# Kernel optimization log

Hardware: AMD Instinct MI355X
Metric: run time of the kernel (lower is better)

Reference implementation:

```python
import jax, jax.numpy as jnp
import numpy as np

B, N, D = 4, 4096, 1024
H = 16
DH = D // H
EPS = 1e-6


def log_map_at_origin(x, c):
    # Poincare ball -> tangent space at origin (matches torch clamps)
    sqrt_c = jnp.sqrt(jnp.maximum(c, 1e-6))
    x_norm = jnp.clip(jnp.linalg.norm(x, axis=-1, keepdims=True), 1e-6, 0.999)
    scale = jnp.arctanh(sqrt_c * x_norm) / (sqrt_c * x_norm + 1e-8)
    return scale * x


def exp_map_at_origin(v, c):
    # tangent space -> Poincare ball
    sqrt_c = jnp.sqrt(jnp.maximum(c, 1e-6))
    v_norm = jnp.clip(jnp.linalg.norm(v, axis=-1, keepdims=True), 1e-6, 15.0)
    tanh_arg = jnp.minimum(sqrt_c * v_norm, 15.0)
    return jnp.tanh(tanh_arg) / (sqrt_c * v_norm + 1e-8) * v


def setup_inputs() -> dict:
    key = jax.random.key(0)
    ks = jax.random.split(key, 9)
    s = 0.02
    return {
        "x": jax.random.normal(ks[0], (B, N, D), jnp.float32),
        "curvature": jnp.asarray(0.05, jnp.float32),  # < low_threshold -> 'linear' mode
        "Wq": jax.random.normal(ks[1], (D, D), jnp.float32) * s,
        "bq": jnp.zeros((D,), jnp.float32),
        "Wk": jax.random.normal(ks[2], (D, D), jnp.float32) * s,
        "bk": jnp.zeros((D,), jnp.float32),
        "Wv": jax.random.normal(ks[3], (D, D), jnp.float32) * s,
        "bv": jnp.zeros((D,), jnp.float32),
        "Wo": jax.random.normal(ks[4], (D, D), jnp.float32) * s,
        "bo": jnp.zeros((D,), jnp.float32),
    }


def reference(x, curvature, Wq, bq, Wk, bk, Wv, bv, Wo, bo):
    c = jnp.maximum(jnp.abs(curvature), 1e-6)
    x_tan = log_map_at_origin(x, c)  # (B,N,D)

    def proj(W, b):
        # torch nn.Linear: y = x W^T + b; split heads -> (B,H,N,Dh)
        return (x_tan @ W.T + b).reshape(B, N, H, DH).transpose(0, 2, 1, 3)

    q = proj(Wq, bq)
    k = proj(Wk, bk)
    v = proj(Wv, bv)

    # KernelFeatureMap, kernel_type='elu': phi(x) = elu(x) + 1
    phi_q = jax.nn.elu(q) + 1.0  # (B,H,N,Dh)
    phi_k = jax.nn.elu(k) + 1.0

    # Linear attention: phi(Q) (phi(K)^T V) / (phi(Q) sum_n phi(K))
    kv = jnp.einsum('bhnd,bhnf->bhfd', v, phi_k)          # (B,H,F,Dh)
    qkv = jnp.einsum('bhnf,bhfd->bhnd', phi_q, kv)        # (B,H,N,Dh)
    k_sum = phi_k.sum(axis=2)                             # (B,H,F)
    normalizer = jnp.maximum(jnp.einsum('bhnf,bhf->bhn', phi_q, k_sum), EPS)
    out = qkv / normalizer[..., None]

    out = out.transpose(0, 2, 1, 3).reshape(B, N, D)
    out = out @ Wo.T + bo
    return exp_map_at_origin(out, c)
```

## Files before the change

### kernel.cpp

```cpp
#include <hip/hip_runtime.h>
#include <cstdint>
#include <cstddef>

#define Bb 4
#define Nn 4096
#define Dd 1024
#define Hh 16
#define ROWS (Bb*Nn)

typedef unsigned short u16;
typedef float    f32x4 __attribute__((ext_vector_type(4)));
typedef _Float16 f16x8 __attribute__((ext_vector_type(8)));
typedef u16      u16x4 __attribute__((ext_vector_type(4)));
typedef u16      u16x8 __attribute__((ext_vector_type(8)));

__device__ inline u16 f2h(float f){ _Float16 h=(_Float16)f; return __builtin_bit_cast(u16,h); }
__device__ inline float h2f(u16 u){ return (float)__builtin_bit_cast(_Float16,u); }

__device__ inline void gl_lds16(const void* g, void* l){
  __builtin_amdgcn_global_load_lds(
      (const __attribute__((address_space(1))) void*)g,
      (__attribute__((address_space(3))) void*)l,
      16, 0, 0);
}

__global__ __launch_bounds__(256) void prep_k(const float* __restrict__ x,
    const float* __restrict__ curv,
    const float* __restrict__ wq, const float* __restrict__ wk,
    const float* __restrict__ wv, const float* __restrict__ wo,
    const float* __restrict__ bq, const float* __restrict__ bk,
    const float* __restrict__ bv,
    u16* __restrict__ xt, u16* __restrict__ wbf, float* __restrict__ bcat)
{
  const int tid = threadIdx.x;
  if (blockIdx.x < ROWS){
    const int row = blockIdx.x;
    const f32x4 v = ((const f32x4*)(x + (size_t)row*Dd))[tid];
    float ss = v[0]*v[0] + v[1]*v[1] + v[2]*v[2] + v[3]*v[3];
    #pragma unroll
    for (int o=32;o>0;o>>=1) ss += __shfl_down(ss, o, 64);
    __shared__ float red[4];
    if ((tid & 63) == 0) red[tid>>6] = ss;
    __syncthreads();
    const float sum = red[0]+red[1]+red[2]+red[3];
    const float c  = fmaxf(fabsf(curv[0]), 1e-6f);
    const float sc = sqrtf(fmaxf(c, 1e-6f));
    const float xn = fminf(fmaxf(sqrtf(sum), 1e-6f), 0.999f);
    const float a  = sc * xn;
    const float scale = atanhf(a) / (a + 1e-8f);
    u16x4 o;
    #pragma unroll
    for (int i=0;i<4;i++) o[i] = f2h(v[i]*scale);
    ((u16x4*)(xt + (size_t)row*Dd))[tid] = o;
  } else {
    const int idx = (blockIdx.x - ROWS)*256 + tid;
    if (idx < (1<<20)){
      const int which = idx >> 18;
      const int rem = idx & ((1<<18)-1);
      const float* src = which==0?wq:which==1?wk:which==2?wv:wo;
      const f32x4 v = ((const f32x4*)src)[rem];
      u16x4 o;
      #pragma unroll
      for (int i=0;i<4;i++) o[i]=f2h(v[i]);
      ((u16x4*)(wbf + (size_t)which*(1u<<20)))[rem] = o;
    } else {
      const int t = idx - (1<<20);
      if (t < 3072)
        bcat[t] = (t<1024) ? bq[t] : (t<2048) ? bk[t-1024] : bv[t-2048];
    }
  }
}

__global__ __launch_bounds__(256) void expmap_k(const u16* __restrict__ proj,
    const float* __restrict__ curv, float* __restrict__ out)
{
  const int row = blockIdx.x, tid = threadIdx.x;
  const u16x4 hv = ((const u16x4*)(proj + (size_t)row*Dd))[tid];
  float v[4];
  #pragma unroll
  for (int i=0;i<4;i++) v[i]=h2f(hv[i]);
  float ss = v[0]*v[0]+v[1]*v[1]+v[2]*v[2]+v[3]*v[3];
  #pragma unroll
  for (int o=32;o>0;o>>=1) ss += __shfl_down(ss,o,64);
  __shared__ float red[4];
  if ((tid&63)==0) red[tid>>6]=ss;
  __syncthreads();
  const float sum = red[0]+red[1]+red[2]+red[3];
  const float c  = fmaxf(fabsf(curv[0]),1e-6f);
  const float sc = sqrtf(fmaxf(c,1e-6f));
  const float vn = fminf(fmaxf(sqrtf(sum),1e-6f),15.0f);
  const float a  = sc*vn;
  const float scale = tanhf(fminf(a,15.0f))/(a + 1e-8f);
  f32x4 o;
  #pragma unroll
  for (int i=0;i<4;i++) o[i]=v[i]*scale;
  ((f32x4*)(out + (size_t)row*Dd))[tid]=o;
}

__global__ __launch_bounds__(512, 1) void gemm8_k(
    const u16* __restrict__ A, const u16* __restrict__ W,
    const float* __restrict__ bias,
    u16* __restrict__ out_n, u16* __restrict__ outT1, u16* __restrict__ outT2,
    int nbn, int phi_modes)
{
  __shared__ __align__(16) char smem[131072];

  const int nwg = gridDim.x;
  const int bid = blockIdx.x;
  const int wgid = (bid & 7)*(nwg >> 3) + (bid >> 3);
  const int bm = wgid / nbn, bn = wgid % nbn;
  const int bm0 = bm*256, bn0 = bn*256;

  const int tid = threadIdx.x;
  const int w = tid >> 6, lane = tid & 63;
  const int wr = w >> 2, wc = w & 3;
  const int l8 = lane >> 3, l7 = lane & 7;

  f32x4 acc[8][4];
  #pragma unroll
  for (int i=0;i<8;i++)
    #pragma unroll
    for (int j=0;j<4;j++) acc[i][j] = (f32x4)(0.f);

  int offA[2][8], offB[2][4];
  #pragma unroll
  for (int ks=0;ks<2;ks++){
    #pragma unroll
    for (int mi=0;mi<8;mi++){
      const int ar = wr*128 + mi*16 + (lane & 15);
      offA[ks][mi] = ar*128 + ((ks*64 + (lane>>4)*16) ^ ((ar & 7) << 4));
    }
    #pragma unroll
    for (int ni=0;ni<4;ni++){
      const int br = wc*64 + ni*16 + (lane & 15);
      offB[ks][ni] = 32768 + br*128 + ((ks*64 + (lane>>4)*16) ^ ((br & 7) << 4));
    }
  }
  const u16* aS[4]; const u16* wS[4]; int dOf[4];
  #pragma unroll
  for (int i=0;i<4;i++){
    const int r = w*32 + i*8 + l8;
    const int cch = l7 ^ (r & 7);
    aS[i] = A + (size_t)(bm0 + r)*Dd + cch*8;
    wS[i] = W + (size_t)(bn0 + r)*Dd + cch*8;
    dOf[i] = (w*32 + i*8)*128;
  }

  auto STAGE = [&](char* base, int kt){
    #pragma unroll
    for (int i=0;i<4;i++){
      gl_lds16(aS[i] + kt*64, base + dOf[i]);
      gl_lds16(wS[i] + kt*64, base + 32768 + dOf[i]);
    }
  };

  auto COMPUTE = [&](const char* base){
    #pragma unroll
    for (int ks=0; ks<2; ks++){
      f16x8 bf[4];
      #pragma unroll
      for (int ni=0; ni<4; ni++)
        bf[ni] = *(const f16x8*)(base + offB[ks][ni]);
      __builtin_amdgcn_s_setprio(1);
      #pragma unroll
      for (int mi=0; mi<8; mi++){
        const f16x8 af = *(const f16x8*)(base + offA[ks][mi]);
        #pragma unroll
        for (int ni=0; ni<4; ni++)
          acc[mi][ni] = __builtin_amdgcn_mfma_f32_16x16x32_f16(af, bf[ni], acc[mi][ni], 0,0,0);
      }
      __builtin_amdgcn_s_setprio(0);
    }
  };

  STAGE(smem, 0);
  __syncthreads();
  #pragma unroll
  for (int p=0; p<8; ++p){
    STAGE(smem + 65536, 2*p+1);
    COMPUTE(smem);
    __syncthreads();
    if (p < 7) STAGE(smem, 2*p+2);
    COMPUTE(smem + 65536);
    __syncthreads();
  }

  const int mode = bn0 >> 10;
  const int dophi = mode < phi_modes;
  if (mode == 1 || mode == 2){
    u16* tbuf = (mode == 1) ? outT1 : outT2;
    char* Ts = smem;
    #pragma unroll
    for (int ni=0;ni<4;ni++){
      const int lcol = wc*64 + ni*16 + (lane & 15);
      const float bs = bias[bn0 + lcol];
      #pragma unroll
      for (int mi=0;mi<8;mi++){
        const int row0 = wr*128 + mi*16 + ((lane>>4)<<2);
        #pragma unroll
        for (int r=0;r<4;r++){
          float val = acc[mi][ni][r] + bs;
          if (dophi) val = val > 0.f ? val + 1.f : __expf(val);
          const int lrow = row0 + r;
          const int bo_ = (lcol*512 + lrow*2) ^ ((lcol&7)<<4);
          *(u16*)(Ts + bo_) = f2h(val);
        }
      }
    }
    __syncthreads();
    {
      const int ch = tid & 31;
      #pragma unroll
      for (int rep=0; rep<16; ++rep){
        const int c = rep*16 + (tid>>5);
        const int bo_ = (c*512 + ch*16) ^ ((c&7)<<4);
        const int mcol = (bn0 & 1023) + c;
        const int h = mcol >> 6, f = mcol & 63;
        const int bh = ((bm0 >> 12) << 4) + h;
        u16* db = tbuf + ((size_t)(bh*64 + f))*Nn + (bm0 & 4095) + ch*8;
        *(u16x8*)db = *(const u16x8*)(Ts + bo_);
      }
    }
  } else {
    u16* Ts = (u16*)smem;
    #pragma unroll
    for (int ni=0;ni<4;ni++){
      const int col = wc*64 + ni*16 + (lane & 15);
      const float bs = bias[bn0 + col];
      #pragma unroll
      for (int mi=0;mi<8;mi++){
        const int row0 = wr*128 + mi*16 + ((lane>>4)<<2);
        #pragma unroll
        for (int r=0;r<4;r++){
          float val = acc[mi][ni][r] + bs;
          if (dophi) val = val > 0.f ? val + 1.f : __expf(val);
          const int row = row0 + r;
          const int bo_ = (row*512 + col*2) ^ ((row&7)<<4);
          *(u16*)((char*)Ts + bo_) = f2h(val);
        }
      }
    }
    __syncthreads();
    #pragma unroll
    for (int j=0;j<16;j++){
      const int row = j*16 + w*2 + (lane>>5);
      const int cb2 = (lane&31)*16;
      const int bo_ = (row*512 + cb2) ^ ((row&7)<<4);
      u16* ob = out_n + (size_t)(bm0 + row)*Dd + (bn0 & 1023) + (cb2>>1);
      *(u16x8*)ob = *(const u16x8*)((const char*)Ts + bo_);
    }
  }
}

__global__ __launch_bounds__(256) void kvmm_k(const u16* __restrict__ pkT,
    const u16* __restrict__ vT, float* __restrict__ pkv, float* __restrict__ pks)
{
  const int p = blockIdx.x, bh = blockIdx.y;
  const int tid = threadIdx.x, w = tid>>6, lane = tid&63;
  __shared__ __align__(16) char smem[65536];
  const size_t abase = (size_t)bh*64*Nn;

  f32x4 acc[5];
  #pragma unroll
  for (int i=0;i<5;i++) acc[i] = (f32x4)(0.f);
  f16x8 onesf;
  #pragma unroll
  for (int i=0;i<8;i++) onesf[i] = (_Float16)1.0f;

  auto STG = [&](int d, int sub){
    char* Ap = smem + d*32768;
    char* Bp = Ap + 16384;
    const int nbase = p*512 + sub*128;
    #pragma unroll
    for (int i=0;i<4;i++){
      const int ib = (w*4+i)*64;
      const int cj = ib + lane;
      const int f = cj>>4, ci = cj&15;
      const size_t off = abase + (size_t)f*Nn + nbase + (ci ^ (f&15))*8;
      gl_lds16(pkT + off, Ap + ib*16);
      gl_lds16(vT  + off, Bp + ib*16);
    }
  };

  auto COMPUTE = [&](int d){
    const char* Ap = smem + d*32768;
    const char* Bp = Ap + 16384;
    #pragma unroll
    for (int s=0; s<4; ++s){
      const int kb = (s*64 + (lane>>4)*16) ^ ((lane&15)<<4);
      const int fr = w*16 + (lane&15);
      const f16x8 af = *(const f16x8*)(Ap + fr*256 + kb);
      #pragma unroll
      for (int ni=0; ni<4; ni++){
        const int dr = ni*16 + (lane&15);
        const f16x8 bf = *(const f16x8*)(Bp + dr*256 + kb);
        acc[ni] = __builtin_amdgcn_mfma_f32_16x16x32_f16(af, bf, acc[ni], 0,0,0);
      }
      acc[4] = __builtin_amdgcn_mfma_f32_16x16x32_f16(af, onesf, acc[4], 0,0,0);
    }
  };

  STG(0, 0);
  __syncthreads();
  for (int sub=0; sub<4; ++sub){
    const int d = sub & 1;
    if (sub < 3) STG(d^1, sub+1);
    COMPUTE(d);
    __syncthreads();
  }

  float* o = pkv + (size_t)(bh*8+p)*4096;
  #pragma unroll
  for (int ni=0;ni<4;ni++)
    #pragma unroll
    for (int r=0;r<4;r++)
      o[(w*16 + ((lane>>4)<<2) + r)*64 + ni*16 + (lane&15)] = acc[ni][r];
  if ((lane&15)==0){
    #pragma unroll
    for (int r=0;r<4;r++)
      pks[(size_t)(bh*8+p)*64 + w*16 + ((lane>>4)<<2) + r] = acc[4][r];
  }
}

__global__ __launch_bounds__(256) void kvred_k(const float* __restrict__ pkv,
    const float* __restrict__ pks, u16* __restrict__ kvt)
{
  const int bh = blockIdx.x, tid = threadIdx.x;
  u16* basep = kvt + (size_t)bh*10240;
  #pragma unroll
  for (int i=0;i<4;i++){
    const int e = tid*16 + i*4;
    f32x4 s = (f32x4)(0.f);
    for (int p=0;p<8;p++)
      s += *(const f32x4*)&pkv[(size_t)(bh*8+p)*4096 + e];
    const int f = e>>6, dd = e&63;
    #pragma unroll
    for (int j=0;j<4;j++){
      const int r = dd+j;
      const u16 hi = f2h(s[j]);
      const int col = f ^ ((r&7)<<3);
      basep[r*64 + col] = hi;
      basep[5120 + r*64 + col] = f2h(s[j] - h2f(hi));
    }
  }
  if (tid < 64){
    float s=0.f;
    for (int p=0;p<8;p++) s += pks[(size_t)(bh*8+p)*64 + tid];
    const u16 hi = f2h(s);
    basep[64*64 + tid] = hi;
    basep[5120 + 64*64 + tid] = f2h(s - h2f(hi));
  }
  if (tid < 240){
    const int r = 65 + (tid>>4), c4 = (tid&15)*4;
    *(u16x4*)&basep[r*64 + c4] = (u16x4)(0);
    *(u16x4*)&basep[5120 + r*64 + c4] = (u16x4)(0);
  }
}

__global__ __launch_bounds__(256) void attn2_k(const u16* __restrict__ phiq,
    const u16* __restrict__ kvt, u16* __restrict__ att)
{
  const int bh = blockIdx.y, b = bh>>4, h = bh&15;
  const int tid = threadIdx.x;
  const int w = tid>>6, lane = tid&63;
  __shared__ __align__(16) u16 kvs[10240];
  __shared__ __align__(16) u16 pqs[2][64*64];

  const int l8 = lane>>3, l7 = lane&7;
  auto STAGE_P = [&](int d, int nt){
    const int n0 = (blockIdx.x*4 + nt)*64;
    const u16* qsrc = phiq + ((size_t)(b*Nn) + n0)*Dd + h*64;
    #pragma unroll
    for (int i=0;i<2;i++){
      const int r = w*16 + i*8 + l8;
      const int cch = l7 ^ (r&7);
      gl_lds16(qsrc + (size_t)r*Dd + cch*8, (char*)pqs[d] + (w*16+i*8)*128);
    }
  };

  {
    const char* src = (const char*)(kvt + (size_t)bh*10240);
    #pragma unroll
    for (int j=0;j<5;j++)
      gl_lds16(src + j*4096 + w*1024 + lane*16, (char*)kvs + j*4096 + w*1024);
    STAGE_P(0, 0);
  }
  __syncthreads();

  #pragma unroll
  for (int nt=0; nt<4; ++nt){
    const int d = nt & 1;
    if (nt < 3) STAGE_P(d^1, nt+1);
    f32x4 acc[5];
    #pragma unroll
    for (int ni=0;ni<5;ni++) acc[ni] = (f32x4)(0.f);
    #pragma unroll
    for (int ks=0; ks<2; ks++){
      const int ar = w*16 + (lane&15);
      const int acb = (ks*64 + (lane>>4)*16) ^ ((ar&7)<<4);
      const f16x8 af = *(const f16x8*)((const char*)pqs[d] + ar*128 + acb);
      #pragma unroll
      for (int ni=0; ni<5; ni++){
        const int br = ni*16 + (lane&15);
        const int bcb = (ks*64 + (lane>>4)*16) ^ ((br&7)<<4);
        const f16x8 bh_ = *(const f16x8*)((const char*)kvs + br*128 + bcb);
        const f16x8 bl_ = *(const f16x8*)((const char*)kvs + 10240 + br*128 + bcb);
        acc[ni] = __builtin_amdgcn_mfma_f32_16x16x32_f16(af, bh_, acc[ni], 0,0,0);
        acc[ni] = __builtin_amdgcn_mfma_f32_16x16x32_f16(af, bl_, acc[ni], 0,0,0);
      }
    }
    const int n0 = (blockIdx.x*4 + nt)*64;
    #pragma unroll
    for (int r=0;r<4;r++){
      const float nrm = __shfl(acc[4][r], (lane & 48), 64);
      const float inv = 1.f / fmaxf(nrm, 1e-6f);
      const int row = n0 + w*16 + ((lane>>4)<<2) + r;
      u16* ob = att + ((size_t)(b*Nn) + row)*Dd + h*64 + (lane&15);
      #pragma unroll
      for (int ni=0; ni<4; ni++)
        ob[ni*16] = f2h(acc[ni][r] * inv);
    }
    __syncthreads();
  }
}

extern "C" void kernel_launch(void* const* d_in, const int* in_sizes, int n_in,
                              void* d_out, int out_size, void* d_ws, size_t ws_size,
                              hipStream_t stream)
{
  const float* x  = (const float*)d_in[0];
  const float* cv = (const float*)d_in[1];
  const float* Wq = (const float*)d_in[2];
  const float* bq = (const float*)d_in[3];
  const float* Wk = (const float*)d_in[4];
  const float* bk = (const float*)d_in[5];
  const float* Wv = (const float*)d_in[6];
  const float* bv = (const float*)d_in[7];
  const float* Wo = (const float*)d_in[8];
  const float* bo = (const float*)d_in[9];
  float* out = (float*)d_out;
  char* ws = (char*)d_ws;
  const size_t MB = 1u<<20;
  if (ws_size < 136*MB) return;

  u16* xt     = (u16*)(ws + 0);
  u16* wbf    = (u16*)(ws + 32*MB);
  u16* phiq   = (u16*)(ws + 40*MB);
  u16* phikT  = (u16*)(ws + 72*MB);
  u16* vT     = (u16*)(ws + 104*MB);
  float* pkv  = (float*)(ws + 0);
  float* pks  = (float*)(ws + 8*MB);
  u16* kvt    = (u16*)(ws + 9*MB);
  u16* att    = (u16*)(ws + 104*MB);
  u16* proj16 = (u16*)(ws + 40*MB);
  float* bcat = out + ((size_t)out_size - 4096);

  prep_k<<<ROWS + 4108, 256, 0, stream>>>(x, cv, Wq, Wk, Wv, Wo, bq, bk, bv,
                                          xt, wbf, bcat);
  gemm8_k<<<768, 512, 0, stream>>>(xt, wbf, bcat, phiq, phikT, vT,
                                   12, 2);
  kvmm_k<<<dim3(8,64), 256, 0, stream>>>(phikT, vT, pkv, pks);
  kvred_k<<<64, 256, 0, stream>>>(pkv, pks, kvt);
  attn2_k<<<dim3(16,64), 256, 0, stream>>>(phiq, kvt, att);
  gemm8_k<<<256, 512, 0, stream>>>(att, wbf + (size_t)3*(1u<<20), bo, proj16,
                                   nullptr, nullptr, 4, 0);
  expmap_k<<<ROWS, 256, 0, stream>>>(proj16, cv, out);
}
```

Baseline: 233.3 us.

## Halve GEMM K-tile and LDS to fit two workgroups per CU, templated N tile

The projection GEMM becomes a template on N-tile width. The K tile per stage drops from 64 to 32 with a new XOR swizzle, so LDS per block halves and launch bounds allow two 512-thread workgroups per CU. The epilogue now stages output through LDS one half-tile at a time so it fits the smaller buffer. The output projection uses a 256x128 tile with 512 blocks to improve load balance. The cost is twice as many barriers per K sweep and tighter register limits, which may cause spills with 32 accumulators per thread.

```diff
diff --git a/kernel.cpp b/kernel.cpp
--- a/kernel.cpp
+++ b/kernel.cpp
@@ -97,157 +97,175 @@
   ((f32x4*)(out + (size_t)row*Dd))[tid]=o;
 }
 
-__global__ __launch_bounds__(512, 1) void gemm8_k(
+template<int NI>
+__global__ __launch_bounds__(512, 2) void gemmN_k(
     const u16* __restrict__ A, const u16* __restrict__ W,
     const float* __restrict__ bias,
     u16* __restrict__ out_n, u16* __restrict__ outT1, u16* __restrict__ outT2,
     int nbn, int phi_modes)
 {
-  __shared__ __align__(16) char smem[131072];
+  constexpr int BN   = NI*64;
+  constexpr int HALF = (256+BN)*64;
+  __shared__ __align__(16) char smem[2*HALF];
 
   const int nwg = gridDim.x;
   const int bid = blockIdx.x;
   const int wgid = (bid & 7)*(nwg >> 3) + (bid >> 3);
   const int bm = wgid / nbn, bn = wgid % nbn;
-  const int bm0 = bm*256, bn0 = bn*256;
+  const int bm0 = bm*256, bn0 = bn*BN;
 
   const int tid = threadIdx.x;
   const int w = tid >> 6, lane = tid & 63;
   const int wr = w >> 2, wc = w & 3;
-  const int l8 = lane >> 3, l7 = lane & 7;
-
-  f32x4 acc[8][4];
+
+  f32x4 acc[8][NI];
   #pragma unroll
   for (int i=0;i<8;i++)
     #pragma unroll
-    for (int j=0;j<4;j++) acc[i][j] = (f32x4)(0.f);
-
-  int offA[2][8], offB[2][4];
-  #pragma unroll
-  for (int ks=0;ks<2;ks++){
-    #pragma unroll
-    for (int mi=0;mi<8;mi++){
-      const int ar = wr*128 + mi*16 + (lane & 15);
-      offA[ks][mi] = ar*128 + ((ks*64 + (lane>>4)*16) ^ ((ar & 7) << 4));
-    }
-    #pragma unroll
-    for (int ni=0;ni<4;ni++){
-      const int br = wc*64 + ni*16 + (lane & 15);
-      offB[ks][ni] = 32768 + br*128 + ((ks*64 + (lane>>4)*16) ^ ((br & 7) << 4));
-    }
-  }
-  const u16* aS[4]; const u16* wS[4]; int dOf[4];
-  #pragma unroll
-  for (int i=0;i<4;i++){
-    const int r = w*32 + i*8 + l8;
-    const int cch = l7 ^ (r & 7);
-    aS[i] = A + (size_t)(bm0 + r)*Dd + cch*8;
-    wS[i] = W + (size_t)(bn0 + r)*Dd + cch*8;
-    dOf[i] = (w*32 + i*8)*128;
+    for (int j=0;j<NI;j++) acc[i][j] = (f32x4)(0.f);
+
+  int offA[8], offB[NI];
+  #pragma unroll
+  for (int mi=0;mi<8;mi++){
+    const int ar = wr*128 + mi*16 + (lane & 15);
+    const int key = (ar ^ (ar>>2)) & 3;
+    offA[mi] = ar*64 + (((lane>>4) ^ key) << 4);
+  }
+  #pragma unroll
+  for (int ni=0;ni<NI;ni++){
+    const int br = wc*(NI*16) + ni*16 + (lane & 15);
+    const int key = (br ^ (br>>2)) & 3;
+    offB[ni] = 16384 + br*64 + (((lane>>4) ^ key) << 4);
+  }
+  const u16* aS[2]; int dofA[2];
+  #pragma unroll
+  for (int j=0;j<2;j++){
+    const int cj = tid + j*512;
+    const int r = cj>>2, sl = cj&3;
+    const int csl = sl ^ ((r ^ (r>>2)) & 3);
+    aS[j] = A + (size_t)(bm0 + r)*Dd + csl*8;
+    dofA[j] = cj*16;
+  }
+  const u16* wS[NI/2]; int dofB[NI/2];
+  #pragma unroll
+  for (int j=0;j<NI/2;j++){
+    const int cj = tid + j*512;
+    const int r = cj>>2, sl = cj&3;
+    const int csl = sl ^ ((r ^ (r>>2)) & 3);
+    wS[j] = W + (size_t)(bn0 + r)*Dd + csl*8;
+    dofB[j] = 16384 + cj*16;
   }
 
   auto STAGE = [&](char* base, int kt){
     #pragma unroll
-    for (int i=0;i<4;i++){
-      gl_lds16(aS[i] + kt*64, base + dOf[i]);
-      gl_lds16(wS[i] + kt*64, base + 32768 + dOf[i]);
-    }
+    for (int j=0;j<2;j++) gl_lds16(aS[j] + kt*32, base + dofA[j]);
+    #pragma unroll
+    for (int j=0;j<NI/2;j++) gl_lds16(wS[j] + kt*32, base + dofB[j]);
   };
 
   auto COMPUTE = [&](const char* base){
-    #pragma unroll
-    for (int ks=0; ks<2; ks++){
-      f16x8 bf[4];
-      #pragma unroll
-      for (int ni=0; ni<4; ni++)
-        bf[ni] = *(const f16x8*)(base + offB[ks][ni]);
-      __builtin_amdgcn_s_setprio(1);
-      #pragma unroll
-      for (int mi=0; mi<8; mi++){
-        const f16x8 af = *(const f16x8*)(base + offA[ks][mi]);
-        #pragma unroll
-        for (int ni=0; ni<4; ni++)
-          acc[mi][ni] = __builtin_amdgcn_mfma_f32_16x16x32_f16(af, bf[ni], acc[mi][ni], 0,0,0);
-      }
-      __builtin_amdgcn_s_setprio(0);
-    }
+    f16x8 bf[NI];
+    #pragma unroll
+    for (int ni=0; ni<NI; ni++)
+      bf[ni] = *(const f16x8*)(base + offB[ni]);
+    __builtin_amdgcn_s_setprio(1);
+    #pragma unroll
+    for (int mi=0; mi<8; mi++){
+      const f16x8 af = *(const f16x8*)(base + offA[mi]);
+      #pragma unroll
+      for (int ni=0; ni<NI; ni++)
+        acc[mi][ni] = __builtin_amdgcn_mfma_f32_16x16x32_f16(af, bf[ni], acc[mi][ni], 0,0,0);
+    }
+    __builtin_amdgcn_s_setprio(0);
   };
 
   STAGE(smem, 0);
   __syncthreads();
   #pragma unroll
-  for (int p=0; p<8; ++p){
-    STAGE(smem + 65536, 2*p+1);
+  for (int p=0; p<16; ++p){
+    STAGE(smem + HALF, 2*p+1);
     COMPUTE(smem);
     __syncthreads();
-    if (p < 7) STAGE(smem, 2*p+2);
-    COMPUTE(smem + 65536);
+    if (p < 15) STAGE(smem, 2*p+2);
+    COMPUTE(smem + HALF);
     __syncthreads();
   }
 
   const int mode = bn0 >> 10;
   const int dophi = mode < phi_modes;
-  if (mode == 1 || mode == 2){
+  if (NI == 4 && mode >= 1){
     u16* tbuf = (mode == 1) ? outT1 : outT2;
     char* Ts = smem;
     #pragma unroll
-    for (int ni=0;ni<4;ni++){
-      const int lcol = wc*64 + ni*16 + (lane & 15);
-      const float bs = bias[bn0 + lcol];
-      #pragma unroll
-      for (int mi=0;mi<8;mi++){
-        const int row0 = wr*128 + mi*16 + ((lane>>4)<<2);
+    for (int half=0; half<2; ++half){
+      if (half) __syncthreads();
+      if (wr == half){
         #pragma unroll
-        for (int r=0;r<4;r++){
-          float val = acc[mi][ni][r] + bs;
-          if (dophi) val = val > 0.f ? val + 1.f : __expf(val);
-          const int lrow = row0 + r;
-          const int bo_ = (lcol*512 + lrow*2) ^ ((lcol&7)<<4);
-          *(u16*)(Ts + bo_) = f2h(val);
+        for (int ni=0;ni<NI;ni++){
+          const int lcol = wc*(NI*16) + ni*16 + (lane & 15);
+          const float bs = bias[bn0 + lcol];
+          #pragma unroll
+          for (int mi=0;mi<8;mi++){
+            const int rl0 = mi*16 + ((lane>>4)<<2);
+            #pragma unroll
+            for (int r=0;r<4;r++){
+              float val = acc[mi][ni][r] + bs;
+              if (dophi) val = val > 0.f ? val + 1.f : __expf(val);
+              const int rl = rl0 + r;
+              const int bo_ = (lcol*256 + rl*2) ^ ((lcol&7)<<4);
+              *(u16*)(Ts + bo_) = f2h(val);
+            }
+          }
         }
       }
-    }
-    __syncthreads();
-    {
-      const int ch = tid & 31;
-      #pragma unroll
-      for (int rep=0; rep<16; ++rep){
-        const int c = rep*16 + (tid>>5);
-        const int bo_ = (c*512 + ch*16) ^ ((c&7)<<4);
-        const int mcol = (bn0 & 1023) + c;
-        const int h = mcol >> 6, f = mcol & 63;
-        const int bh = ((bm0 >> 12) << 4) + h;
-        u16* db = tbuf + ((size_t)(bh*64 + f))*Nn + (bm0 & 4095) + ch*8;
-        *(u16x8*)db = *(const u16x8*)(Ts + bo_);
+      __syncthreads();
+      {
+        const int ch = tid & 15;
+        #pragma unroll
+        for (int rep=0; rep<8; ++rep){
+          const int c = rep*32 + (tid>>4);
+          const int bo_ = (c*256 + ch*16) ^ ((c&7)<<4);
+          const int mcol = (bn0 & 1023) + c;
+          const int h = mcol >> 6, f = mcol & 63;
+          const int bh = ((bm0 >> 12) << 4) + h;
+          u16* db = tbuf + ((size_t)(bh*64 + f))*Nn + (bm0 & 4095) + half*128 + ch*8;
+          *(u16x8*)db = *(const u16x8*)(Ts + bo_);
+        }
       }
     }
   } else {
     u16* Ts = (u16*)smem;
     #pragma unroll
-    for (int ni=0;ni<4;ni++){
-      const int col = wc*64 + ni*16 + (lane & 15);
-      const float bs = bias[bn0 + col];
-      #pragma unroll
-      for (int mi=0;mi<8;mi++){
-        const int row0 = wr*128 + mi*16 + ((lane>>4)<<2);
+    for (int half=0; half<2; ++half){
+      if (half) __syncthreads();
+      if (wr == half){
         #pragma unroll
-        for (int r=0;r<4;r++){
-          float val = acc[mi][ni][r] + bs;
-          if (dophi) val = val > 0.f ? val + 1.f : __expf(val);
-          const int row = row0 + r;
-          const int bo_ = (row*512 + col*2) ^ ((row&7)<<4);
-          *(u16*)((char*)Ts + bo_) = f2h(val);
+        for (int ni=0;ni<NI;ni++){
+          const int col = wc*(NI*16) + ni*16 + (lane & 15);
+          const float bs = bias[bn0 + col];
+          #pragma unroll
+          for (int mi=0;mi<8;mi++){
+            const int rl0 = mi*16 + ((lane>>4)<<2);
+            #pragma unroll
+            for (int r=0;r<4;r++){
+              float val = acc[mi][ni][r] + bs;
+              if (dophi) val = val > 0.f ? val + 1.f : __expf(val);
+              const int rl = rl0 + r;
+              const int bo_ = (rl*(BN*2) + col*2) ^ ((rl&7)<<4);
+              *(u16*)((char*)Ts + bo_) = f2h(val);
+            }
+          }
         }
       }
-    }
-    __syncthreads();
-    #pragma unroll
-    for (int j=0;j<16;j++){
-      const int row = j*16 + w*2 + (lane>>5);
-      const int cb2 = (lane&31)*16;
-      const int bo_ = (row*512 + cb2) ^ ((row&7)<<4);
-      u16* ob = out_n + (size_t)(bm0 + row)*Dd + (bn0 & 1023) + (cb2>>1);
-      *(u16x8*)ob = *(const u16x8*)((const char*)Ts + bo_);
+      __syncthreads();
+      #pragma unroll
+      for (int t=0; t<NI*2; ++t){
+        const int c = tid + t*512;
+        const int rl = c / (BN/8), wch = c % (BN/8);
+        const int bo_ = (rl*(BN*2) + wch*16) ^ ((rl&7)<<4);
+        u16* ob = out_n + (size_t)(bm0 + half*128 + rl)*Dd + (bn0 & 1023) + wch*8;
+        *(u16x8*)ob = *(const u16x8*)((const char*)Ts + bo_);
+      }
     }
   }
 }
@@ -457,12 +475,12 @@
 
   prep_k<<<ROWS + 4108, 256, 0, stream>>>(x, cv, Wq, Wk, Wv, Wo, bq, bk, bv,
                                           xt, wbf, bcat);
-  gemm8_k<<<768, 512, 0, stream>>>(xt, wbf, bcat, phiq, phikT, vT,
-                                   12, 2);
+  gemmN_k<4><<<768, 512, 0, stream>>>(xt, wbf, bcat, phiq, phikT, vT,
+                                      12, 2);
   kvmm_k<<<dim3(8,64), 256, 0, stream>>>(phikT, vT, pkv, pks);
   kvred_k<<<64, 256, 0, stream>>>(pkv, pks, kvt);
   attn2_k<<<dim3(16,64), 256, 0, stream>>>(phiq, kvt, att);
-  gemm8_k<<<256, 512, 0, stream>>>(att, wbf + (size_t)3*(1u<<20), bo, proj16,
-                                   nullptr, nullptr, 4, 0);
+  gemmN_k<2><<<512, 512, 0, stream>>>(att, wbf + (size_t)3*(1u<<20), bo, proj16,
+                                      nullptr, nullptr, 8, 0);
   expmap_k<<<ROWS, 256, 0, stream>>>(proj16, cv, out);
 }
```

Measured after the change: 267.0 us. 1.14x slower.

## Add single-buffered half-LDS QKV GEMM variant to fit two workgroups per CU

Applied to the files above, without the earlier changes.

Adds a QKV projection GEMM that uses 64KB of LDS with a single buffer instead of 128KB double-buffered, and sets launch bounds to two workgroups per CU. Latency is meant to be hidden by running two resident workgroups rather than by software pipelining. The epilogue is split into two halves by wave row so the transpose staging fits in the smaller LDS. The output-projection GEMM keeps the old double-buffered kernel with the phi and transpose paths stripped. Risks: more register pressure under the two-block bound, which could cause spills of the 128-float accumulator, plus extra barriers and no overlap of loads with compute inside a block.

```diff
diff --git a/kernel.cpp b/kernel.cpp
--- a/kernel.cpp
+++ b/kernel.cpp
@@ -97,13 +97,13 @@
   ((f32x4*)(out + (size_t)row*Dd))[tid]=o;
 }
 
-__global__ __launch_bounds__(512, 1) void gemm8_k(
+__global__ __launch_bounds__(512, 2) void gemmS_k(
     const u16* __restrict__ A, const u16* __restrict__ W,
     const float* __restrict__ bias,
     u16* __restrict__ out_n, u16* __restrict__ outT1, u16* __restrict__ outT2,
     int nbn, int phi_modes)
 {
-  __shared__ __align__(16) char smem[131072];
+  __shared__ __align__(16) char smem[65536];
 
   const int nwg = gridDim.x;
   const int bid = blockIdx.x;
@@ -146,6 +146,168 @@
     dOf[i] = (w*32 + i*8)*128;
   }
 
+  auto STAGE = [&](int kt){
+    #pragma unroll
+    for (int i=0;i<4;i++){
+      gl_lds16(aS[i] + kt*64, smem + dOf[i]);
+      gl_lds16(wS[i] + kt*64, smem + 32768 + dOf[i]);
+    }
+  };
+
+  auto COMPUTE = [&](){
+    #pragma unroll
+    for (int ks=0; ks<2; ks++){
+      f16x8 bf[4];
+      #pragma unroll
+      for (int ni=0; ni<4; ni++)
+        bf[ni] = *(const f16x8*)(smem + offB[ks][ni]);
+      __builtin_amdgcn_s_setprio(1);
+      #pragma unroll
+      for (int mi=0; mi<8; mi++){
+        const f16x8 af = *(const f16x8*)(smem + offA[ks][mi]);
+        #pragma unroll
+        for (int ni=0; ni<4; ni++)
+          acc[mi][ni] = __builtin_amdgcn_mfma_f32_16x16x32_f16(af, bf[ni], acc[mi][ni], 0,0,0);
+      }
+      __builtin_amdgcn_s_setprio(0);
+    }
+  };
+
+  #pragma unroll
+  for (int kt=0; kt<16; ++kt){
+    STAGE(kt);
+    __syncthreads();
+    COMPUTE();
+    __syncthreads();
+  }
+
+  const int mode = bn0 >> 10;
+  const int dophi = mode < phi_modes;
+  if (mode >= 1){
+    u16* tbuf = (mode == 1) ? outT1 : outT2;
+    char* Ts = smem;
+    #pragma unroll
+    for (int half=0; half<2; ++half){
+      if (half) __syncthreads();
+      if (wr == half){
+        #pragma unroll
+        for (int ni=0;ni<4;ni++){
+          const int lcol = wc*64 + ni*16 + (lane & 15);
+          const float bs = bias[bn0 + lcol];
+          #pragma unroll
+          for (int mi=0;mi<8;mi++){
+            const int rl0 = mi*16 + ((lane>>4)<<2);
+            #pragma unroll
+            for (int r=0;r<4;r++){
+              float val = acc[mi][ni][r] + bs;
+              if (dophi) val = val > 0.f ? val + 1.f : __expf(val);
+              const int rl = rl0 + r;
+              const int bo_ = (lcol*256 + rl*2) ^ ((lcol&7)<<4);
+              *(u16*)(Ts + bo_) = f2h(val);
+            }
+          }
+        }
+      }
+      __syncthreads();
+      {
+        const int ch = tid & 15;
+        #pragma unroll
+        for (int rep=0; rep<8; ++rep){
+          const int c = rep*32 + (tid>>4);
+          const int bo_ = (c*256 + ch*16) ^ ((c&7)<<4);
+          const int mcol = (bn0 & 1023) + c;
+          const int h = mcol >> 6, f = mcol & 63;
+          const int bh = ((bm0 >> 12) << 4) + h;
+          u16* db = tbuf + ((size_t)(bh*64 + f))*Nn + (bm0 & 4095) + half*128 + ch*8;
+          *(u16x8*)db = *(const u16x8*)(Ts + bo_);
+        }
+      }
+    }
+  } else {
+    u16* Ts = (u16*)smem;
+    #pragma unroll
+    for (int half=0; half<2; ++half){
+      if (half) __syncthreads();
+      if (wr == half){
+        #pragma unroll
+        for (int ni=0;ni<4;ni++){
+          const int col = wc*64 + ni*16 + (lane & 15);
+          const float bs = bias[bn0 + col];
+          #pragma unroll
+          for (int mi=0;mi<8;mi++){
+            const int rl0 = mi*16 + ((lane>>4)<<2);
+            #pragma unroll
+            for (int r=0;r<4;r++){
+              float val = acc[mi][ni][r] + bs;
+              if (dophi) val = val > 0.f ? val + 1.f : __expf(val);
+              const int rl = rl0 + r;
+              const int bo_ = (rl*512 + col*2) ^ ((rl&7)<<4);
+              *(u16*)((char*)Ts + bo_) = f2h(val);
+            }
+          }
+        }
+      }
+      __syncthreads();
+      #pragma unroll
+      for (int t=0; t<8; ++t){
+        const int c = tid + t*512;
+        const int rl = c >> 5, wch = c & 31;
+        const int bo_ = (rl*512 + wch*16) ^ ((rl&7)<<4);
+        u16* ob = out_n + (size_t)(bm0 + half*128 + rl)*Dd + (bn0 & 1023) + wch*8;
+        *(u16x8*)ob = *(const u16x8*)((const char*)Ts + bo_);
+      }
+    }
+  }
+}
+
+__global__ __launch_bounds__(512, 1) void gemm8_k(
+    const u16* __restrict__ A, const u16* __restrict__ W,
+    const float* __restrict__ bias,
+    u16* __restrict__ out_n, int nbn)
+{
+  __shared__ __align__(16) char smem[131072];
+
+  const int nwg = gridDim.x;
+  const int bid = blockIdx.x;
+  const int wgid = (bid & 7)*(nwg >> 3) + (bid >> 3);
+  const int bm = wgid / nbn, bn = wgid % nbn;
+  const int bm0 = bm*256, bn0 = bn*256;
+
+  const int tid = threadIdx.x;
+  const int w = tid >> 6, lane = tid & 63;
+  const int wr = w >> 2, wc = w & 3;
+  const int l8 = lane >> 3, l7 = lane & 7;
+
+  f32x4 acc[8][4];
+  #pragma unroll
+  for (int i=0;i<8;i++)
+    #pragma unroll
+    for (int j=0;j<4;j++) acc[i][j] = (f32x4)(0.f);
+
+  int offA[2][8], offB[2][4];
+  #pragma unroll
+  for (int ks=0;ks<2;ks++){
+    #pragma unroll
+    for (int mi=0;mi<8;mi++){
+      const int ar = wr*128 + mi*16 + (lane & 15);
+      offA[ks][mi] = ar*128 + ((ks*64 + (lane>>4)*16) ^ ((ar & 7) << 4));
+    }
+    #pragma unroll
+    for (int ni=0;ni<4;ni++){
+      const int br = wc*64 + ni*16 + (lane & 15);
+      offB[ks][ni] = 32768 + br*128 + ((ks*64 + (lane>>4)*16) ^ ((br & 7) << 4));
+    }
+  }
+  const u16* aS[4]; const u16* wS[4]; int dOf[4];
+  #pragma unroll
+  for (int i=0;i<4;i++){
+    const int r = w*32 + i*8 + l8;
+    const int cch = l7 ^ (r & 7);
+    aS[i] = A + (size_t)(bm0 + r)*Dd + cch*8;
+    wS[i] = W + (size_t)(bn0 + r)*Dd + cch*8;
+    dOf[i] = (w*32 + i*8)*128;
+  }
+
   auto STAGE = [&](char* base, int kt){
     #pragma unroll
     for (int i=0;i<4;i++){
@@ -185,70 +347,31 @@
     __syncthreads();
   }
 
-  const int mode = bn0 >> 10;
-  const int dophi = mode < phi_modes;
-  if (mode == 1 || mode == 2){
-    u16* tbuf = (mode == 1) ? outT1 : outT2;
-    char* Ts = smem;
-    #pragma unroll
-    for (int ni=0;ni<4;ni++){
-      const int lcol = wc*64 + ni*16 + (lane & 15);
-      const float bs = bias[bn0 + lcol];
-      #pragma unroll
-      for (int mi=0;mi<8;mi++){
-        const int row0 = wr*128 + mi*16 + ((lane>>4)<<2);
-        #pragma unroll
-        for (int r=0;r<4;r++){
-          float val = acc[mi][ni][r] + bs;
-          if (dophi) val = val > 0.f ? val + 1.f : __expf(val);
-          const int lrow = row0 + r;
-          const int bo_ = (lcol*512 + lrow*2) ^ ((lcol&7)<<4);
-          *(u16*)(Ts + bo_) = f2h(val);
-        }
-      }
-    }
-    __syncthreads();
-    {
-      const int ch = tid & 31;
-      #pragma unroll
-      for (int rep=0; rep<16; ++rep){
-        const int c = rep*16 + (tid>>5);
-        const int bo_ = (c*512 + ch*16) ^ ((c&7)<<4);
-        const int mcol = (bn0 & 1023) + c;
-        const int h = mcol >> 6, f = mcol & 63;
-        const int bh = ((bm0 >> 12) << 4) + h;
-        u16* db = tbuf + ((size_t)(bh*64 + f))*Nn + (bm0 & 4095) + ch*8;
-        *(u16x8*)db = *(const u16x8*)(Ts + bo_);
-      }
-    }
-  } else {
-    u16* Ts = (u16*)smem;
-    #pragma unroll
-    for (int ni=0;ni<4;ni++){
-      const int col = wc*64 + ni*16 + (lane & 15);
-      const float bs = bias[bn0 + col];
-      #pragma unroll
-      for (int mi=0;mi<8;mi++){
-        const int row0 = wr*128 + mi*16 + ((lane>>4)<<2);
-        #pragma unroll
-        for (int r=0;r<4;r++){
-          float val = acc[mi][ni][r] + bs;
-          if (dophi) val = val > 0.f ? val + 1.f : __expf(val);
-          const int row = row0 + r;
-          const int bo_ = (row*512 + col*2) ^ ((row&7)<<4);
-          *(u16*)((char*)Ts + bo_) = f2h(val);
-        }
-      }
-    }
-    __syncthreads();
-    #pragma unroll
-    for (int j=0;j<16;j++){
-      const int row = j*16 + w*2 + (lane>>5);
-      const int cb2 = (lane&31)*16;
-      const int bo_ = (row*512 + cb2) ^ ((row&7)<<4);
-      u16* ob = out_n + (size_t)(bm0 + row)*Dd + (bn0 & 1023) + (cb2>>1);
-      *(u16x8*)ob = *(const u16x8*)((const char*)Ts + bo_);
-    }
+  u16* Ts = (u16*)smem;
+  #pragma unroll
+  for (int ni=0;ni<4;ni++){
+    const int col = wc*64 + ni*16 + (lane & 15);
+    const float bs = bias[bn0 + col];
+    #pragma unroll
+    for (int mi=0;mi<8;mi++){
+      const int row0 = wr*128 + mi*16 + ((lane>>4)<<2);
+      #pragma unroll
+      for (int r=0;r<4;r++){
+        const float val = acc[mi][ni][r] + bs;
+        const int row = row0 + r;
+        const int bo_ = (row*512 + col*2) ^ ((row&7)<<4);
+        *(u16*)((char*)Ts + bo_) = f2h(val);
+      }
+    }
+  }
+  __syncthreads();
+  #pragma unroll
+  for (int j=0;j<16;j++){
+    const int row = j*16 + w*2 + (lane>>5);
+    const int cb2 = (lane&31)*16;
+    const int bo_ = (row*512 + cb2) ^ ((row&7)<<4);
+    u16* ob = out_n + (size_t)(bm0 + row)*Dd + (bn0 & 1023) + (cb2>>1);
+    *(u16x8*)ob = *(const u16x8*)((const char*)Ts + bo_);
   }
 }
 
@@ -457,12 +580,11 @@
 
   prep_k<<<ROWS + 4108, 256, 0, stream>>>(x, cv, Wq, Wk, Wv, Wo, bq, bk, bv,
                                           xt, wbf, bcat);
-  gemm8_k<<<768, 512, 0, stream>>>(xt, wbf, bcat, phiq, phikT, vT,
+  gemmS_k<<<768, 512, 0, stream>>>(xt, wbf, bcat, phiq, phikT, vT,
                                    12, 2);
   kvmm_k<<<dim3(8,64), 256, 0, stream>>>(phikT, vT, pkv, pks);
   kvred_k<<<64, 256, 0, stream>>>(pkv, pks, kvt);
   attn2_k<<<dim3(16,64), 256, 0, stream>>>(phiq, kvt, att);
-  gemm8_k<<<256, 512, 0, stream>>>(att, wbf + (size_t)3*(1u<<20), bo, proj16,
-                                   nullptr, nullptr, 4, 0);
+  gemm8_k<<<256, 512, 0, stream>>>(att, wbf + (size_t)3*(1u<<20), bo, proj16, 4);
   expmap_k<<<ROWS, 256, 0, stream>>>(proj16, cv, out);
 }
```

Measured after the change: 266.7 us. 1.14x slower.

## Software-pipeline QKV GEMM with fine-grained half-tile staging and split barriers

Applied to the files above, without the earlier changes.

The QKV projection GEMM is rewritten into an 8-phase schedule. Each phase loads a quarter of the A fragments, issues one half-tile global-to-LDS copy, and runs a slice of MFMAs, with explicit vmcnt waits and raw s_barriers replacing the coarse per-tile __syncthreads. This aims to overlap memory traffic with matrix work more evenly and hide load latency. The output GEMM keeps the old kernel under a trimmed signature. The hand-tuned waitcnt ordering risks subtle races if the staging order is wrong.

```diff
diff --git a/kernel.cpp b/kernel.cpp
--- a/kernel.cpp
+++ b/kernel.cpp
@@ -97,7 +97,7 @@
   ((f32x4*)(out + (size_t)row*Dd))[tid]=o;
 }
 
-__global__ __launch_bounds__(512, 1) void gemm8_k(
+__global__ __launch_bounds__(512, 1) void gemm8p_k(
     const u16* __restrict__ A, const u16* __restrict__ W,
     const float* __restrict__ bias,
     u16* __restrict__ out_n, u16* __restrict__ outT1, u16* __restrict__ outT2,
@@ -114,75 +114,88 @@
   const int tid = threadIdx.x;
   const int w = tid >> 6, lane = tid & 63;
   const int wr = w >> 2, wc = w & 3;
-  const int l8 = lane >> 3, l7 = lane & 7;
 
   f32x4 acc[8][4];
   #pragma unroll
   for (int i=0;i<8;i++)
     #pragma unroll
     for (int j=0;j<4;j++) acc[i][j] = (f32x4)(0.f);
-
-  int offA[2][8], offB[2][4];
-  #pragma unroll
-  for (int ks=0;ks<2;ks++){
-    #pragma unroll
-    for (int mi=0;mi<8;mi++){
-      const int ar = wr*128 + mi*16 + (lane & 15);
-      offA[ks][mi] = ar*128 + ((ks*64 + (lane>>4)*16) ^ ((ar & 7) << 4));
-    }
-    #pragma unroll
-    for (int ni=0;ni<4;ni++){
-      const int br = wc*64 + ni*16 + (lane & 15);
-      offB[ks][ni] = 32768 + br*128 + ((ks*64 + (lane>>4)*16) ^ ((br & 7) << 4));
-    }
-  }
-  const u16* aS[4]; const u16* wS[4]; int dOf[4];
-  #pragma unroll
-  for (int i=0;i<4;i++){
-    const int r = w*32 + i*8 + l8;
-    const int cch = l7 ^ (r & 7);
-    aS[i] = A + (size_t)(bm0 + r)*Dd + cch*8;
-    wS[i] = W + (size_t)(bn0 + r)*Dd + cch*8;
-    dOf[i] = (w*32 + i*8)*128;
-  }
-
-  auto STAGE = [&](char* base, int kt){
-    #pragma unroll
-    for (int i=0;i<4;i++){
-      gl_lds16(aS[i] + kt*64, base + dOf[i]);
-      gl_lds16(wS[i] + kt*64, base + 32768 + dOf[i]);
+  f16x8 bfc[2][4];
+
+  auto STG = [&](int d, int mat, int h, int kt){
+    char* base = smem + d*65536 + mat*32768 + h*16384;
+    const u16* srcb = mat ? (W + (size_t)bn0*Dd) : (A + (size_t)bm0*Dd);
+    #pragma unroll
+    for (int j=0;j<2;j++){
+      const int cj = w*128 + j*64 + lane;
+      const int r = cj>>3, ch = cj&7;
+      const int cch = ch ^ (r&7);
+      gl_lds16(srcb + (size_t)(h*128 + r)*Dd + kt*64 + cch*8, base + cj*16);
     }
   };
 
-  auto COMPUTE = [&](const char* base){
-    #pragma unroll
-    for (int ks=0; ks<2; ks++){
-      f16x8 bf[4];
-      #pragma unroll
-      for (int ni=0; ni<4; ni++)
-        bf[ni] = *(const f16x8*)(base + offB[ks][ni]);
+  STG(0,0,0,0); STG(0,0,1,0); STG(0,1,0,0); STG(0,1,1,0);
+  STG(1,1,0,1); STG(1,1,1,1);
+  asm volatile("s_waitcnt vmcnt(4)" ::: "memory");
+  __builtin_amdgcn_s_barrier();
+
+  #pragma unroll 1
+  for (int it=0; it<8; ++it){
+    const int te = 2*it;
+    #pragma unroll
+    for (int ph=0; ph<8; ++ph){
+      const int d = ph>>2, p4 = ph&3;
+      const char* Ab = smem + d*65536;
+      const char* Bbp = smem + d*65536 + 32768;
+      if (p4 == 0){
+        #pragma unroll
+        for (int ks=0;ks<2;ks++)
+          #pragma unroll
+          for (int ni=0;ni<4;ni++){
+            const int br = wc*64 + ni*16 + (lane&15);
+            const int cb = (ks*64 + ((lane>>4)<<4)) ^ ((br&7)<<4);
+            bfc[ks][ni] = *(const f16x8*)(Bbp + br*128 + cb);
+          }
+      }
+      f16x8 af[2][2];
+      #pragma unroll
+      for (int dm=0;dm<2;dm++)
+        #pragma unroll
+        for (int ks=0;ks<2;ks++){
+          const int ar = wr*128 + (p4*2+dm)*16 + (lane&15);
+          const int cb = (ks*64 + ((lane>>4)<<4)) ^ ((ar&7)<<4);
+          af[dm][ks] = *(const f16x8*)(Ab + ar*128 + cb);
+        }
+      if (ph == 0) STG(1,0,0, te+1);
+      else if (ph == 1) STG(1,0,1, te+1);
+      else if (it < 7){
+        if      (ph == 2) STG(0,1,0, te+2);
+        else if (ph == 3) STG(0,1,1, te+2);
+        else if (ph == 4) STG(0,0,0, te+2);
+        else if (ph == 5) STG(0,0,1, te+2);
+        else if (ph == 6) STG(1,1,0, te+3);
+        else              STG(1,1,1, te+3);
+      }
+      __builtin_amdgcn_s_barrier();
+      asm volatile("s_waitcnt lgkmcnt(0)" ::: "memory");
       __builtin_amdgcn_s_setprio(1);
       #pragma unroll
-      for (int mi=0; mi<8; mi++){
-        const f16x8 af = *(const f16x8*)(base + offA[ks][mi]);
+      for (int ks=0;ks<2;ks++)
         #pragma unroll
-        for (int ni=0; ni<4; ni++)
-          acc[mi][ni] = __builtin_amdgcn_mfma_f32_16x16x32_f16(af, bf[ni], acc[mi][ni], 0,0,0);
-      }
+        for (int dm=0;dm<2;dm++)
+          #pragma unroll
+          for (int ni=0;ni<4;ni++)
+            acc[p4*2+dm][ni] = __builtin_amdgcn_mfma_f32_16x16x32_f16(
+                af[dm][ks], bfc[ks][ni], acc[p4*2+dm][ni], 0,0,0);
       __builtin_amdgcn_s_setprio(0);
-    }
-  };
-
-  STAGE(smem, 0);
-  __syncthreads();
-  #pragma unroll
-  for (int p=0; p<8; ++p){
-    STAGE(smem + 65536, 2*p+1);
-    COMPUTE(smem);
-    __syncthreads();
-    if (p < 7) STAGE(smem, 2*p+2);
-    COMPUTE(smem + 65536);
-    __syncthreads();
+      if (ph == 3){
+        if (it < 7) asm volatile("s_waitcnt vmcnt(4)" ::: "memory");
+        else        asm volatile("s_waitcnt vmcnt(0)" ::: "memory");
+      } else if (ph == 7 && it < 7){
+        asm volatile("s_waitcnt vmcnt(4)" ::: "memory");
+      }
+      __builtin_amdgcn_s_barrier();
+    }
   }
 
   const int mode = bn0 >> 10;
@@ -249,6 +262,121 @@
       u16* ob = out_n + (size_t)(bm0 + row)*Dd + (bn0 & 1023) + (cb2>>1);
       *(u16x8*)ob = *(const u16x8*)((const char*)Ts + bo_);
     }
+  }
+}
+
+__global__ __launch_bounds__(512, 1) void gemm8_k(
+    const u16* __restrict__ A, const u16* __restrict__ W,
+    const float* __restrict__ bias,
+    u16* __restrict__ out_n, int nbn)
+{
+  __shared__ __align__(16) char smem[131072];
+
+  const int nwg = gridDim.x;
+  const int bid = blockIdx.x;
+  const int wgid = (bid & 7)*(nwg >> 3) + (bid >> 3);
+  const int bm = wgid / nbn, bn = wgid % nbn;
+  const int bm0 = bm*256, bn0 = bn*256;
+
+  const int tid = threadIdx.x;
+  const int w = tid >> 6, lane = tid & 63;
+  const int wr = w >> 2, wc = w & 3;
+  const int l8 = lane >> 3, l7 = lane & 7;
+
+  f32x4 acc[8][4];
+  #pragma unroll
+  for (int i=0;i<8;i++)
+    #pragma unroll
+    for (int j=0;j<4;j++) acc[i][j] = (f32x4)(0.f);
+
+  int offA[2][8], offB[2][4];
+  #pragma unroll
+  for (int ks=0;ks<2;ks++){
+    #pragma unroll
+    for (int mi=0;mi<8;mi++){
+      const int ar = wr*128 + mi*16 + (lane & 15);
+      offA[ks][mi] = ar*128 + ((ks*64 + (lane>>4)*16) ^ ((ar & 7) << 4));
+    }
+    #pragma unroll
+    for (int ni=0;ni<4;ni++){
+      const int br = wc*64 + ni*16 + (lane & 15);
+      offB[ks][ni] = 32768 + br*128 + ((ks*64 + (lane>>4)*16) ^ ((br & 7) << 4));
+    }
+  }
+  const u16* aS[4]; const u16* wS[4]; int dOf[4];
+  #pragma unroll
+  for (int i=0;i<4;i++){
+    const int r = w*32 + i*8 + l8;
+    const int cch = l7 ^ (r & 7);
+    aS[i] = A + (size_t)(bm0 + r)*Dd + cch*8;
+    wS[i] = W + (size_t)(bn0 + r)*Dd + cch*8;
+    dOf[i] = (w*32 + i*8)*128;
+  }
+
+  auto STAGE = [&](char* base, int kt){
+    #pragma unroll
+    for (int i=0;i<4;i++){
+      gl_lds16(aS[i] + kt*64, base + dOf[i]);
+      gl_lds16(wS[i] + kt*64, base + 32768 + dOf[i]);
+    }
+  };
+
+  auto COMPUTE = [&](const char* base){
+    #pragma unroll
+    for (int ks=0; ks<2; ks++){
+      f16x8 bf[4];
+      #pragma unroll
+      for (int ni=0; ni<4; ni++)
+        bf[ni] = *(const f16x8*)(base + offB[ks][ni]);
+      __builtin_amdgcn_s_setprio(1);
+      #pragma unroll
+      for (int mi=0; mi<8; mi++){
+        const f16x8 af = *(const f16x8*)(base + offA[ks][mi]);
+        #pragma unroll
+        for (int ni=0; ni<4; ni++)
+          acc[mi][ni] = __builtin_amdgcn_mfma_f32_16x16x32_f16(af, bf[ni], acc[mi][ni], 0,0,0);
+      }
+      __builtin_amdgcn_s_setprio(0);
+    }
+  };
+
+  STAGE(smem, 0);
+  __syncthreads();
+  #pragma unroll
+  for (int p=0; p<8; ++p){
+    STAGE(smem + 65536, 2*p+1);
+    COMPUTE(smem);
+    __syncthreads();
+    if (p < 7) STAGE(smem, 2*p+2);
+    COMPUTE(smem + 65536);
+    __syncthreads();
+  }
+
+  u16* Ts = (u16*)smem;
+  #pragma unroll
+  for (int ni=0;ni<4;ni++){
+    const int col = wc*64 + ni*16 + (lane & 15);
+    const float bs = bias[bn0 + col];
+    #pragma unroll
+    for (int mi=0;mi<8;mi++){
+      const int row0 = wr*128 + mi*16 + ((lane>>4)<<2);
+      #pragma unroll
+      for (int r=0;r<4;r++){
+        const float val = acc[mi][ni][r] + bs;
+        const int row = row0 + r;
+        const int bo_ = (row*512 + col*2) ^ ((row&7)<<4);
+        *(u16*)((char*)Ts + bo_) = f2h(val);
+      }
+    }
+  }
+  __syncthreads();
+  #pragma unroll
+  for (int j=0;j<16;j++){
+    const int row = j*16 + w*2 + (lane>>5);
+    const int cb2 = (lane&31)*16;
+    const int bo_ = (row*512 + cb2) ^ ((row&7)<<4);
+    u16* ob = out_n + (size_t)(bm0 + row)*Dd + (bn0 & 1023) + (cb2>>1);
+    *(u16x8*)ob = *(const u16x8*)((const char*)Ts + bo_);
   }
 }
 
@@ -457,12 +585,11 @@
 
   prep_k<<<ROWS + 4108, 256, 0, stream>>>(x, cv, Wq, Wk, Wv, Wo, bq, bk, bv,
                                           xt, wbf, bcat);
-  gemm8_k<<<768, 512, 0, stream>>>(xt, wbf, bcat, phiq, phikT, vT,
-                                   12, 2);
+  gemm8p_k<<<768, 512, 0, stream>>>(xt, wbf, bcat, phiq, phikT, vT,
+                                    12, 2);
   kvmm_k<<<dim3(8,64), 256, 0, stream>>>(phikT, vT, pkv, pks);
   kvred_k<<<64, 256, 0, stream>>>(pkv, pks, kvt);
   attn2_k<<<dim3(16,64), 256, 0, stream>>>(phiq, kvt, att);
-  gemm8_k<<<256, 512, 0, stream>>>(att, wbf + (size_t)3*(1u<<20), bo, proj16,
-                                   nullptr, nullptr, 4, 0);
+  gemm8_k<<<256, 512, 0, stream>>>(att, wbf + (size_t)3*(1u<<20), bo, proj16, 4);
   expmap_k<<<ROWS, 256, 0, stream>>>(proj16, cv, out);
 }
```

Result: no change. 236.6 us (+1.4%).
